# Performance work log

Measured on AMD Instinct MI355X. Metric: run time of the kernel, lower is better.

Reference implementation:

```python
import jax, jax.numpy as jnp
import numpy as np

SPECIES = [1, 6, 7, 8]
N_SPECIES = len(SPECIES)
MAX_Z = max(SPECIES) + 1  # 9
N_IN = 256
N_HIDDEN = 512
N_OUT = 1
N_ATOMS = 65536


def setup_inputs() -> dict:
    key = jax.random.key(0)
    ks = jax.random.split(key, 9)
    x = jax.random.normal(ks[0], (N_ATOMS, N_IN), dtype=jnp.float32)
    z = jax.random.randint(ks[1], (N_ATOMS,), 0, MAX_Z)
    s = 0.05
    # Stacked per-species MLP parameters: [S, ...]
    W1 = jax.random.normal(ks[2], (N_SPECIES, N_HIDDEN, N_IN), dtype=jnp.float32) * s
    b1 = jax.random.normal(ks[3], (N_SPECIES, N_HIDDEN), dtype=jnp.float32) * s
    W2 = jax.random.normal(ks[4], (N_SPECIES, N_HIDDEN, N_HIDDEN), dtype=jnp.float32) * s
    b2 = jax.random.normal(ks[5], (N_SPECIES, N_HIDDEN), dtype=jnp.float32) * s
    W3 = jax.random.normal(ks[6], (N_SPECIES, N_OUT, N_HIDDEN), dtype=jnp.float32) * s
    b3 = jax.random.normal(ks[7], (N_SPECIES, N_OUT), dtype=jnp.float32) * s
    # One-hot embedding table [MAX_Z, N_SPECIES]: row Z has 1.0 at its species slot
    E = np.zeros((MAX_Z, N_SPECIES), dtype=np.float32)
    for idx, Z in enumerate(SPECIES):
        E[Z, idx] = 1.0
    E = jnp.asarray(E)
    return {"x": x, "z": z, "W1": W1, "b1": b1, "W2": W2, "b2": b2,
            "W3": W3, "b3": b3, "E": E}


def reference(x, z, W1, b1, W2, b2, W3, b3, E):
    # Every atom runs through all species MLPs (dense, O(N*S)), as in the original.
    # h1: [N, S, H]
    h1 = jnp.tanh(jnp.einsum('ni,shi->nsh', x, W1) + b1[None])
    h2 = jnp.tanh(jnp.einsum('nsh,sgh->nsg', h1, W2) + b2[None])
    # out_s: [N, S, n_out] -> [N, S*n_out] (n_out == 1 -> [N, S])
    out_s = (jnp.einsum('nsh,soh->nso', h2, W3) + b3[None]).reshape(x.shape[0], -1)
    gate = E[z]  # [N, S] embedding lookup (one-hot hard routing)
    return jnp.sum(out_s * gate, axis=1)  # [N]
```

## Files before the change

kernel.cpp:

```cpp
#include <hip/hip_runtime.h>

typedef __attribute__((ext_vector_type(8))) short bf16x8;
typedef __attribute__((ext_vector_type(4))) float f32x4;
typedef __attribute__((ext_vector_type(2))) unsigned int u32x2;
typedef unsigned short us;

#define NATOMS 65536
#define NIN 256
#define NHID 512
#define TM 64
#define LDB 528

__device__ __forceinline__ us f2b(float f) {
    union { float f; unsigned int u; } a; a.f = f;
    unsigned int r = a.u + 0x7FFFu + ((a.u >> 16) & 1u);
    return (us)(r >> 16);
}
__device__ __forceinline__ float fast_tanh(float v) {
    float t = __builtin_amdgcn_exp2f(v * 2.88539008f);
    float r = __builtin_amdgcn_rcpf(t + 1.f);
    return __builtin_fmaf(-2.f, r, 1.f);
}
__device__ __forceinline__ unsigned cvt_pk(float lo, float hi) {
    unsigned p;
    asm("v_cvt_pk_bf16_f32 %0, %1, %2" : "=v"(p) : "v"(lo), "v"(hi));
    return p;
}

__global__ void cvt_kernel(const float* __restrict__ W1, const float* __restrict__ W2,
                           const float* __restrict__ W3,
                           us* __restrict__ W1p, us* __restrict__ W2p,
                           us* __restrict__ W3b) {
    int i = blockIdx.x * blockDim.x + threadIdx.x;
    if (i < 65536) {
        int s = i >> 14, rem = i & 16383;
        int ntile = rem >> 9, r2 = rem & 511;
        int kstep = r2 >> 6, lane = r2 & 63;
        int n = ntile * 16 + (lane & 15);
        int k = kstep * 32 + ((lane >> 4) << 3);
        const float* src = W1 + ((size_t)(s * NHID + n) * NIN + k);
        us p[8];
#pragma unroll
        for (int j = 0; j < 8; ++j) p[j] = f2b(src[j]);
        *(uint4*)(W1p + (size_t)i * 8) = *(uint4*)p;
    }
    if (i < 131072) {
        int s = i >> 15, rem = i & 32767;
        int ntile = rem >> 10, r2 = rem & 1023;
        int kstep = r2 >> 6, lane = r2 & 63;
        int n = ntile * 16 + (lane & 15);
        int k = kstep * 32 + ((lane >> 4) << 3);
        const float* src = W2 + ((size_t)(s * NHID + n) * NHID + k);
        us p[8];
#pragma unroll
        for (int j = 0; j < 8; ++j) p[j] = f2b(src[j]);
        *(uint4*)(W2p + (size_t)i * 8) = *(uint4*)p;
    }
    if (i < 2048) W3b[i] = f2b(W3[i]);
}

__global__ __launch_bounds__(1024) void compact_kernel(
    const int* __restrict__ z, int* __restrict__ cnt,
    int* __restrict__ lists, float* __restrict__ out) {
    __shared__ int lcnt[4];
    __shared__ int gbase[4];
    __shared__ int wbase[16][4];

    int tid = threadIdx.x;
    int wv = tid >> 6;
    int lane = tid & 63;
    if (tid < 4) lcnt[tid] = 0;
    __syncthreads();

    int i = blockIdx.x * 1024 + tid;
    int zz = z[i];
    int s = (zz == 1) ? 0 : (zz == 6) ? 1 : (zz == 7) ? 2 : (zz == 8) ? 3 : -1;
    if (s < 0) out[i] = 0.f;

    int prefix = 0;
#pragma unroll
    for (int sp = 0; sp < 4; ++sp) {
        unsigned long long m = __ballot(s == sp);
        if (m) {
            int c = __popcll(m);
            int leader = __ffsll((long long)m) - 1;
            if (lane == leader) wbase[wv][sp] = atomicAdd(&lcnt[sp], c);
            if (s == sp) prefix = __popcll(m & ((1ull << lane) - 1ull));
        }
    }
    __syncthreads();
    if (tid < 4) gbase[tid] = atomicAdd(&cnt[tid], lcnt[tid]);
    __syncthreads();

    if (s >= 0) lists[s * NATOMS + gbase[s] + wbase[wv][s] + prefix] = i;
}

template<int K>
__device__ __forceinline__ void gemm4(const char* ldsLo, const char* ldsHi, const us* Wp,
                                      int lane, int wtile, f32x4 acc[4][4]) {
    constexpr int KS = K / 32;
    const us* wp[4];
#pragma unroll
    for (int nt = 0; nt < 4; ++nt)
        wp[nt] = Wp + (((size_t)(wtile + nt) * KS) * 64 + lane) * 8;
    int aoff[4];
#pragma unroll
    for (int mt = 0; mt < 4; ++mt)
        aoff[mt] = (mt * 16 + (lane & 15)) * LDB + (((lane >> 4) << 3) << 1);

    bf16x8 a[2][4], b[2][4];
#pragma unroll
    for (int mt = 0; mt < 4; ++mt) a[0][mt] = *(const bf16x8*)(ldsLo + aoff[mt]);
#pragma unroll
    for (int nt = 0; nt < 4; ++nt) b[0][nt] = *(const bf16x8*)wp[nt];

#pragma unroll
    for (int i = 0; i < KS; ++i) {
        const int cur = i & 1, nxt = cur ^ 1;
        if (i + 1 < KS) {
            const int j = i + 1;
            const char* src = (j < 8) ? (ldsLo + j * 64) : (ldsHi + (j - 8) * 64);
#pragma unroll
            for (int mt = 0; mt < 4; ++mt)
                a[nxt][mt] = *(const bf16x8*)(src + aoff[mt]);
#pragma unroll
            for (int nt = 0; nt < 4; ++nt)
                b[nxt][nt] = *(const bf16x8*)(wp[nt] + j * 512);
        }
#pragma unroll
        for (int nt = 0; nt < 4; ++nt)
#pragma unroll
            for (int mt = 0; mt < 4; ++mt)
                acc[mt][nt] = __builtin_amdgcn_mfma_f32_16x16x32_bf16(a[cur][mt], b[cur][nt], acc[mt][nt], 0, 0, 0);
    }
}

__device__ __forceinline__ void act_store_split(char* bufA, char* bufB,
                                                const float* __restrict__ bias,
                                                int lane, int ncb, f32x4 acc[4][4]) {
    char* dstBase = (ncb < 256) ? bufA : bufB;
    int coff = (ncb < 256) ? ncb : (ncb - 256);
#pragma unroll
    for (int nt = 0; nt < 4; ++nt) {
        int nl = coff + nt * 16 + (lane & 15);
        float bv = bias[ncb + nt * 16 + (lane & 15)];
#pragma unroll
        for (int mt = 0; mt < 4; ++mt) {
            float t0 = fast_tanh(acc[mt][nt][0] + bv);
            float t1 = fast_tanh(acc[mt][nt][1] + bv);
            float t2 = fast_tanh(acc[mt][nt][2] + bv);
            float t3 = fast_tanh(acc[mt][nt][3] + bv);
            unsigned p01 = cvt_pk(t0, t1);
            unsigned p23 = cvt_pk(t2, t3);
            int row0 = mt * 16 + ((lane >> 4) << 2);
            char* base = dstBase + row0 * LDB + nl * 2;
            *(us*)(base)           = (us)p01;
            *(us*)(base + LDB)     = (us)(p01 >> 16);
            *(us*)(base + 2 * LDB) = (us)p23;
            *(us*)(base + 3 * LDB) = (us)(p23 >> 16);
        }
    }
}

__global__ __launch_bounds__(512, 2) void mlp_kernel(
    const float* __restrict__ x, const int* __restrict__ cnt, const int* __restrict__ lists,
    const us* __restrict__ W1p, const us* __restrict__ W2p, const us* __restrict__ W3b,
    const float* __restrict__ b1, const float* __restrict__ b2, const float* __restrict__ b3,
    float* __restrict__ out) {
    int bx = blockIdx.x;
    int s = bx & 3;
    int t = bx >> 2;
    int base = t * TM;
    int n_s = cnt[s];
    if (base >= n_s) return;
    const int* list = lists + s * NATOMS;
    int cnt_t = n_s - base; if (cnt_t > TM) cnt_t = TM;

    __shared__ __align__(16) char bufA[TM * LDB];
    __shared__ __align__(16) char bufB[TM * LDB];

    int tid = threadIdx.x;
    int lane = tid & 63;
    int w = tid >> 6;
    int wtile = w * 4;
    int ncb = w * 64;

    {
        int r = tid >> 3;
        int cb = (tid & 7) * 32;
        int atom = (r < cnt_t) ? list[base + r] : -1;
        const float* xr = x + (size_t)(atom < 0 ? 0 : atom) * NIN;
#pragma unroll
        for (int j = 0; j < 8; ++j) {
            int c = cb + j * 4;
            float4 v;
            if (atom >= 0) v = *(const float4*)(xr + c);
            else v = make_float4(0.f, 0.f, 0.f, 0.f);
            u32x2 p;
            p.x = cvt_pk(v.x, v.y);
            p.y = cvt_pk(v.z, v.w);
            *(u32x2*)(bufB + r * LDB + c * 2) = p;
        }
    }
    __syncthreads();

    {
        f32x4 acc[4][4];
#pragma unroll
        for (int i = 0; i < 4; ++i)
#pragma unroll
            for (int j = 0; j < 4; ++j) acc[i][j] = (f32x4){0.f, 0.f, 0.f, 0.f};
        gemm4<NIN>(bufB, bufB, W1p + (size_t)s * NHID * NIN, lane, wtile, acc);
        __syncthreads();
        act_store_split(bufA, bufB, b1 + s * NHID, lane, ncb, acc);
    }
    __syncthreads();

    {
        f32x4 acc[4][4];
#pragma unroll
        for (int i = 0; i < 4; ++i)
#pragma unroll
            for (int j = 0; j < 4; ++j) acc[i][j] = (f32x4){0.f, 0.f, 0.f, 0.f};
        gemm4<NHID>(bufA, bufB, W2p + (size_t)s * NHID * NHID, lane, wtile, acc);
        __syncthreads();
        act_store_split(bufA, bufB, b2 + s * NHID, lane, ncb, acc);
    }
    __syncthreads();

    {
        int m = tid >> 3;
        int q = tid & 7;
        const us* W3s = W3b + (size_t)s * NHID;
        const char* src = (q < 4) ? bufA : bufB;
        int cbase = (q < 4) ? q * 64 : q * 64 - 256;
        float sum = 0.f;
#pragma unroll
        for (int j = 0; j < 8; ++j) {
            int hh = cbase + j * 8;
            bf16x8 hv = *(const bf16x8*)(src + m * LDB + hh * 2);
            bf16x8 wv = *(const bf16x8*)(W3s + q * 64 + j * 8);
#pragma unroll
            for (int e = 0; e < 8; ++e) {
                union { unsigned u; float f; } ha, wa;
                ha.u = ((unsigned)(us)hv[e]) << 16;
                wa.u = ((unsigned)(us)wv[e]) << 16;
                sum += ha.f * wa.f;
            }
        }
        sum += __shfl_xor(sum, 1);
        sum += __shfl_xor(sum, 2);
        sum += __shfl_xor(sum, 4);
        if (q == 0 && m < cnt_t) out[list[base + m]] = sum + b3[s];
    }
}

extern "C" void kernel_launch(void* const* d_in, const int* in_sizes, int n_in,
                              void* d_out, int out_size, void* d_ws, size_t ws_size,
                              hipStream_t stream) {
    const float* x  = (const float*)d_in[0];
    const int*   z  = (const int*)d_in[1];
    const float* W1 = (const float*)d_in[2];
    const float* b1 = (const float*)d_in[3];
    const float* W2 = (const float*)d_in[4];
    const float* b2 = (const float*)d_in[5];
    const float* W3 = (const float*)d_in[6];
    const float* b3 = (const float*)d_in[7];
    float* out = (float*)d_out;

    char* ws = (char*)d_ws;
    int* cnt = (int*)ws;
    int* lists = (int*)(ws + 256);
    us* W1p = (us*)(ws + 256 + (size_t)4 * NATOMS * 4);
    us* W2p = W1p + 4 * NHID * NIN;
    us* W3b = W2p + 4 * NHID * NHID;

    (void)hipMemsetAsync(cnt, 0, 16, stream);
    cvt_kernel<<<512, 256, 0, stream>>>(W1, W2, W3, W1p, W2p, W3b);
    compact_kernel<<<NATOMS / 1024, 1024, 0, stream>>>(z, cnt, lists, out);
    mlp_kernel<<<4096, 512, 0, stream>>>(x, cnt, lists, W1p, W2p, W3b, b1, b2, b3, out);
}
```

Baseline: 66.35 us.

## Double MLP atom tile to 128 rows with a 2x8 wave grid per block

Each block now handles 128 atoms with 1024 threads, arranged as 16 waves in a 2x8 grid, so every weight fragment loaded from global memory serves twice as many rows. The LDS A-operand double buffering is replaced by loading A fragments inside each k-step, which lowers register pressure. The cost is that the two activation buffers grow to about 135KB of LDS per block, allowing only one block per CU. The launch bound of (1024, 2) may also squeeze the per-thread register budget enough to force spills of the accumulators. Larger tiles also leave more padded rows in the last tile of each species.

```diff
diff --git a/kernel.cpp b/kernel.cpp
--- a/kernel.cpp
+++ b/kernel.cpp
@@ -8,7 +8,7 @@
 #define NATOMS 65536
 #define NIN 256
 #define NHID 512
-#define TM 64
+#define TM 128
 #define LDB 528
 
 __device__ __forceinline__ us f2b(float f) {
@@ -96,8 +96,8 @@
 }
 
 template<int K>
-__device__ __forceinline__ void gemm4(const char* ldsLo, const char* ldsHi, const us* Wp,
-                                      int lane, int wtile, f32x4 acc[4][4]) {
+__device__ __forceinline__ void gemm4w(const char* ldsLo, const char* ldsHi, const us* Wp,
+                                       int lane, int rbase, int wtile, f32x4 acc[4][4]) {
     constexpr int KS = K / 32;
     const us* wp[4];
 #pragma unroll
@@ -106,11 +106,9 @@
     int aoff[4];
 #pragma unroll
     for (int mt = 0; mt < 4; ++mt)
-        aoff[mt] = (mt * 16 + (lane & 15)) * LDB + (((lane >> 4) << 3) << 1);
-
-    bf16x8 a[2][4], b[2][4];
-#pragma unroll
-    for (int mt = 0; mt < 4; ++mt) a[0][mt] = *(const bf16x8*)(ldsLo + aoff[mt]);
+        aoff[mt] = (rbase + mt * 16 + (lane & 15)) * LDB + (((lane >> 4) << 3) << 1);
+
+    bf16x8 b[2][4];
 #pragma unroll
     for (int nt = 0; nt < 4; ++nt) b[0][nt] = *(const bf16x8*)wp[nt];
 
@@ -118,26 +116,26 @@
     for (int i = 0; i < KS; ++i) {
         const int cur = i & 1, nxt = cur ^ 1;
         if (i + 1 < KS) {
-            const int j = i + 1;
-            const char* src = (j < 8) ? (ldsLo + j * 64) : (ldsHi + (j - 8) * 64);
+#pragma unroll
+            for (int nt = 0; nt < 4; ++nt)
+                b[nxt][nt] = *(const bf16x8*)(wp[nt] + (i + 1) * 512);
+        }
+        const char* src = (i < 8) ? (ldsLo + i * 64) : (ldsHi + (i - 8) * 64);
+        bf16x8 a[4];
+#pragma unroll
+        for (int mt = 0; mt < 4; ++mt)
+            a[mt] = *(const bf16x8*)(src + aoff[mt]);
+#pragma unroll
+        for (int nt = 0; nt < 4; ++nt)
 #pragma unroll
             for (int mt = 0; mt < 4; ++mt)
-                a[nxt][mt] = *(const bf16x8*)(src + aoff[mt]);
-#pragma unroll
-            for (int nt = 0; nt < 4; ++nt)
-                b[nxt][nt] = *(const bf16x8*)(wp[nt] + j * 512);
-        }
-#pragma unroll
-        for (int nt = 0; nt < 4; ++nt)
-#pragma unroll
-            for (int mt = 0; mt < 4; ++mt)
-                acc[mt][nt] = __builtin_amdgcn_mfma_f32_16x16x32_bf16(a[cur][mt], b[cur][nt], acc[mt][nt], 0, 0, 0);
+                acc[mt][nt] = __builtin_amdgcn_mfma_f32_16x16x32_bf16(a[mt], b[cur][nt], acc[mt][nt], 0, 0, 0);
     }
 }
 
 __device__ __forceinline__ void act_store_split(char* bufA, char* bufB,
                                                 const float* __restrict__ bias,
-                                                int lane, int ncb, f32x4 acc[4][4]) {
+                                                int lane, int rbase, int ncb, f32x4 acc[4][4]) {
     char* dstBase = (ncb < 256) ? bufA : bufB;
     int coff = (ncb < 256) ? ncb : (ncb - 256);
 #pragma unroll
@@ -152,7 +150,7 @@
             float t3 = fast_tanh(acc[mt][nt][3] + bv);
             unsigned p01 = cvt_pk(t0, t1);
             unsigned p23 = cvt_pk(t2, t3);
-            int row0 = mt * 16 + ((lane >> 4) << 2);
+            int row0 = rbase + mt * 16 + ((lane >> 4) << 2);
             char* base = dstBase + row0 * LDB + nl * 2;
             *(us*)(base)           = (us)p01;
             *(us*)(base + LDB)     = (us)(p01 >> 16);
@@ -162,7 +160,7 @@
     }
 }
 
-__global__ __launch_bounds__(512, 2) void mlp_kernel(
+__global__ __launch_bounds__(1024, 2) void mlp_kernel(
     const float* __restrict__ x, const int* __restrict__ cnt, const int* __restrict__ lists,
     const us* __restrict__ W1p, const us* __restrict__ W2p, const us* __restrict__ W3b,
     const float* __restrict__ b1, const float* __restrict__ b2, const float* __restrict__ b3,
@@ -182,8 +180,11 @@
     int tid = threadIdx.x;
     int lane = tid & 63;
     int w = tid >> 6;
-    int wtile = w * 4;
-    int ncb = w * 64;
+    int wm = w >> 3;
+    int wn = w & 7;
+    int rbase = wm * 64;
+    int wtile = wn * 4;
+    int ncb = wn * 64;
 
     {
         int r = tid >> 3;
@@ -210,9 +211,9 @@
         for (int i = 0; i < 4; ++i)
 #pragma unroll
             for (int j = 0; j < 4; ++j) acc[i][j] = (f32x4){0.f, 0.f, 0.f, 0.f};
-        gemm4<NIN>(bufB, bufB, W1p + (size_t)s * NHID * NIN, lane, wtile, acc);
+        gemm4w<NIN>(bufB, bufB, W1p + (size_t)s * NHID * NIN, lane, rbase, wtile, acc);
         __syncthreads();
-        act_store_split(bufA, bufB, b1 + s * NHID, lane, ncb, acc);
+        act_store_split(bufA, bufB, b1 + s * NHID, lane, rbase, ncb, acc);
     }
     __syncthreads();
 
@@ -222,9 +223,9 @@
         for (int i = 0; i < 4; ++i)
 #pragma unroll
             for (int j = 0; j < 4; ++j) acc[i][j] = (f32x4){0.f, 0.f, 0.f, 0.f};
-        gemm4<NHID>(bufA, bufB, W2p + (size_t)s * NHID * NHID, lane, wtile, acc);
+        gemm4w<NHID>(bufA, bufB, W2p + (size_t)s * NHID * NHID, lane, rbase, wtile, acc);
         __syncthreads();
-        act_store_split(bufA, bufB, b2 + s * NHID, lane, ncb, acc);
+        act_store_split(bufA, bufB, b2 + s * NHID, lane, rbase, ncb, acc);
     }
     __syncthreads();
 
@@ -278,5 +279,5 @@
     (void)hipMemsetAsync(cnt, 0, 16, stream);
     cvt_kernel<<<512, 256, 0, stream>>>(W1, W2, W3, W1p, W2p, W3b);
     compact_kernel<<<NATOMS / 1024, 1024, 0, stream>>>(z, cnt, lists, out);
-    mlp_kernel<<<4096, 512, 0, stream>>>(x, cnt, lists, W1p, W2p, W3b, b1, b2, b3, out);
-}
+    mlp_kernel<<<2048, 1024, 0, stream>>>(x, cnt, lists, W1p, W2p, W3b, b1, b2, b3, out);
+}
```

Result: slower. 81.23 us (+22.4%).
